# Optimization experiments

Hardware: AMD Instinct MI355X
Metric: run time of the kernel (lower is better)

Reference implementation:

```python
import jax, jax.numpy as jnp
import numpy as np
from jax import lax

ANG_RES = 9
MINDISP = -4
MAXDISP = 4
DN = ('NCHW', 'OIHW', 'NCHW')


def _dilat_pad(d, ang):
    if d < 0:
        dilat = abs(d) * ang + 1
        pad = (ang * (ang - 1) * abs(d)) // 2
    elif d == 0:
        dilat = 1
        pad = 0
    else:
        dilat = abs(d) * ang - 1
        pad = (ang * (ang - 1) * abs(d)) // 2 - ang + 1
    return dilat, pad


def setup_inputs() -> dict:
    key = jax.random.key(0)
    k1, k2 = jax.random.split(key)
    x = jax.random.normal(k1, (4, 64, 432, 432), dtype=jnp.float32)  # [B, Cin, angRes*H, angRes*W]
    W = jax.random.normal(k2, (64, 64, 9, 9), dtype=jnp.float32) * 0.05  # [Cout, Cin, angRes, angRes]
    return {"x": x, "W": W}


def reference(x, W):
    costs = []
    for d in range(MINDISP, MAXDISP + 1):
        dilat, pad = _dilat_pad(d, ANG_RES)
        cost = lax.conv_general_dilated(
            x, W,
            window_strides=(ANG_RES, ANG_RES),
            padding=[(pad, pad), (pad, pad)],
            rhs_dilation=(dilat, dilat),
            dimension_numbers=DN,
        )  # [B, Cout, H, W]
        costs.append(cost)
    # stack along new disparity axis -> [B, Cout, D, H, W]
    return jnp.stack(costs, axis=2)
```

## Files before the change

### kernel.cpp

```cpp
#include <hip/hip_runtime.h>

#define ANG 9
#define OHW 48
#define IMG 432
#define CIN 64
#define COUT 64
#define ND 9
#define NB 4
#define NVIEW 81
#define NSPAT 2304
#define NTOT 9216

#define SLABW 81
#define SLABSZ (80 * SLABW)

using f32x4 = __attribute__((ext_vector_type(4))) float;
using s16x8 = __attribute__((ext_vector_type(8))) short;

__device__ __forceinline__ unsigned short f2bf(float f) {
    unsigned u = __float_as_uint(f);
    unsigned r = (u + 0x7FFFu + ((u >> 16) & 1u)) >> 16;
    return (unsigned short)r;
}

__global__ void k_wpack(const float* __restrict__ w, unsigned short* __restrict__ aw) {
    int idx = blockIdx.x * 256 + threadIdx.x;
    if (idx >= NVIEW * 128 * 64) return;
    int ci = idx & 63;
    int m  = (idx >> 6) & 127;
    int uv = idx >> 13;
    int u = uv / 9, v = uv % 9;
    int co = m & 63, var = m >> 6;
    int uu = var ? 8 - u : u;
    int vv = var ? 8 - v : v;
    aw[idx] = f2bf(w[((size_t)(co * 64 + ci) * 9 + uu) * 9 + vv]);
}

__global__ __launch_bounds__(512, 4)
void k_fused(const float* __restrict__ x,
             const unsigned short* __restrict__ aw,
             unsigned short* __restrict__ y) {
    __shared__ unsigned short lx[IMG * 64];
    const int h = blockIdx.x, u = blockIdx.y, b = blockIdx.z;
    const int t = threadIdx.x;
    const int ih = 9 * h + u;
    const int lane = t & 63, wave = t >> 6;
    const int lr = lane & 15;
    const int lh = lane >> 4;
    const int mh = wave >> 2;
    const int mf = wave & 3;

    const unsigned short* abase =
        aw + (((size_t)(u * 9) * 128) + mh * 64 + mf * 16 + lr) * 64 + lh * 8;
    s16x8 a0[9];
#pragma unroll
    for (int v = 0; v < 9; ++v)
        a0[v] = *reinterpret_cast<const s16x8*>(abase + (size_t)v * 128 * 64);

    {
        const int tx = t & 127, ty = t >> 7;
        if (tx < 108) {
            const float* base = x + (((size_t)b * 64) * IMG + ih) * IMG + 4 * tx;
#pragma unroll 4
            for (int k = 0; k < 16; ++k) {
                const int ci = ty * 16 + k;
                const float4 v4 = *reinterpret_cast<const float4*>(
                    base + (size_t)ci * (IMG * IMG));
                unsigned short us[4] = {f2bf(v4.x), f2bf(v4.y), f2bf(v4.z), f2bf(v4.w)};
#pragma unroll
                for (int jj = 0; jj < 4; ++jj) {
                    const int iw = 4 * tx + jj;
                    const int sc = ci ^ (((iw >> 2) & 7) << 3);
                    lx[iw * 64 + sc] = us[jj];
                }
            }
        }
    }
    __syncthreads();

#pragma unroll
    for (int v = 0; v < 9; ++v) {
        const int uv = u * 9 + v;
        const s16x8 a1 = *reinterpret_cast<const s16x8*>(
            abase + (size_t)v * 128 * 64 + 32);
#pragma unroll
        for (int nt = 0; nt < 3; ++nt) {
            const int iw = 9 * (nt * 16 + lr) + v;
            const int g  = (iw >> 2) & 7;
            const s16x8 b0 = *reinterpret_cast<const s16x8*>(&lx[iw * 64 + ((lh ^ g) * 8)]);
            const s16x8 b1 = *reinterpret_cast<const s16x8*>(&lx[iw * 64 + (((4 + lh) ^ g) * 8)]);

            f32x4 acc = (f32x4){0.f, 0.f, 0.f, 0.f};
            acc = __builtin_amdgcn_mfma_f32_16x16x32_bf16(a0[v], b0, acc, 0, 0, 0);
            acc = __builtin_amdgcn_mfma_f32_16x16x32_bf16(a1,    b1, acc, 0, 0, 0);

            const int n0 = b * NSPAT + h * 48 + nt * 16;
#pragma unroll
            for (int rr = 0; rr < 4; ++rr) {
                const int m = mh * 64 + mf * 16 + lh * 4 + rr;
                y[((size_t)uv * 128 + m) * NTOT + n0 + lr] = f2bf(acc[rr]);
            }
        }
    }
}

__global__ __launch_bounds__(576)
void k_gather4(const unsigned short* __restrict__ y, float* __restrict__ out) {
    __shared__ float lds[2 * SLABSZ];
    const int co = blockIdx.x, b = blockIdx.y;
    const int tid = threadIdx.x;

    for (int i = tid; i < 2 * SLABSZ; i += 576) lds[i] = 0.f;

    const int var  = tid / 288;
    const int e0   = (tid % 288) * 8;
    const int srow = e0 / 48, scol = e0 % 48;
    const int ldst = var * SLABSZ + (16 + srow) * SLABW + 16 + scol;
    const unsigned short* ybase =
        y + ((size_t)(var * 64 + co)) * NTOT + (size_t)b * NSPAT + e0;

    const int hh = tid / 12;
    const int w0 = (tid % 12) * 4;
    const int center = (16 + hh) * SLABW + 16 + w0;

    float acc[9][4];
#pragma unroll
    for (int dd = 0; dd < 9; ++dd)
#pragma unroll
        for (int i = 0; i < 4; ++i) acc[dd][i] = 0.f;

    uint4 pre0 = *reinterpret_cast<const uint4*>(ybase);
    uint4 pre1 = *reinterpret_cast<const uint4*>(ybase + (size_t)128 * NTOT);
    __syncthreads();

    for (int uv = 0; uv < NVIEW; ++uv) {
        float4 lo, hi;
        lo.x = __uint_as_float(pre0.x << 16);
        lo.y = __uint_as_float(pre0.x & 0xffff0000u);
        lo.z = __uint_as_float(pre0.y << 16);
        lo.w = __uint_as_float(pre0.y & 0xffff0000u);
        hi.x = __uint_as_float(pre0.z << 16);
        hi.y = __uint_as_float(pre0.z & 0xffff0000u);
        hi.z = __uint_as_float(pre0.w << 16);
        hi.w = __uint_as_float(pre0.w & 0xffff0000u);
        *reinterpret_cast<float4*>(&lds[ldst])     = lo;
        *reinterpret_cast<float4*>(&lds[ldst + 4]) = hi;

        pre0 = pre1;
        if (uv + 2 < NVIEW)
            pre1 = *reinterpret_cast<const uint4*>(ybase + (size_t)(uv + 2) * 128 * NTOT);

        __syncthreads();

        const int uq = uv / 9, vq = uv % 9;
        const int step = (uq - 4) * SLABW + (vq - 4);
        int base = center + 4 * step;
#pragma unroll
        for (int dd = 0; dd < 9; ++dd) {
            const float* p = &lds[base + (dd > 4 ? SLABSZ : 0)];
            acc[dd][0] += p[0];
            acc[dd][1] += p[1];
            acc[dd][2] += p[2];
            acc[dd][3] += p[3];
            base -= step;
        }
        __syncthreads();
    }

    const size_t ob = (size_t)(b * 64 + co) * 9 * NSPAT + tid * 4;
#pragma unroll
    for (int dd = 0; dd < 9; ++dd) {
        float4 o;
        o.x = acc[dd][0]; o.y = acc[dd][1]; o.z = acc[dd][2]; o.w = acc[dd][3];
        *reinterpret_cast<float4*>(&out[ob + (size_t)dd * NSPAT]) = o;
    }
}

__global__ __launch_bounds__(192)
void cost_volume_direct(const float* __restrict__ x,
                        const float* __restrict__ w,
                        float* __restrict__ out) {
    const int ow      = threadIdx.x;
    const int oh      = blockIdx.y * 4 + threadIdx.y;
    const int co_tile = blockIdx.x & 7;
    const int dd      = blockIdx.x >> 3;
    const int b       = blockIdx.z;
    const int d       = dd - 4;
    const int co0     = co_tile * 8;

    int dilat, pad;
    if (d < 0)       { dilat = (-d) * ANG + 1; pad = 36 * (-d); }
    else if (d == 0) { dilat = 1;              pad = 0; }
    else             { dilat = d * ANG - 1;    pad = 36 * d - (ANG - 1); }

    const int ih0 = oh * ANG - pad;
    const int iw0 = ow * ANG - pad;

    float acc[8];
#pragma unroll
    for (int i = 0; i < 8; ++i) acc[i] = 0.f;

    const float* xb = x + (size_t)b * CIN * IMG * IMG;
    for (int kh = 0; kh < ANG; ++kh) {
        const int ih = ih0 + kh * dilat;
        if ((unsigned)ih >= (unsigned)IMG) continue;
        const float* xrow_base = xb + (size_t)ih * IMG;
        const float* wrow      = w + kh * ANG;
        for (int ci = 0; ci < CIN; ++ci) {
            const float* xrow = xrow_base + (size_t)ci * (IMG * IMG);
            float xv[ANG];
#pragma unroll
            for (int kw = 0; kw < ANG; ++kw) {
                const int iw  = iw0 + kw * dilat;
                const bool ok = ((unsigned)iw < (unsigned)IMG);
                const float vv = xrow[ok ? iw : 0];
                xv[kw] = ok ? vv : 0.f;
            }
            const float* wc = wrow + ci * (ANG * ANG);
#pragma unroll
            for (int i = 0; i < 8; ++i) {
                const float* wi = wc + (size_t)(co0 + i) * (CIN * ANG * ANG);
#pragma unroll
                for (int kw = 0; kw < ANG; ++kw)
                    acc[i] = fmaf(xv[kw], wi[kw], acc[i]);
            }
        }
    }
#pragma unroll
    for (int i = 0; i < 8; ++i) {
        const size_t o = ((((size_t)b * COUT + (co0 + i)) * ND + dd) * OHW + oh) * OHW + ow;
        out[o] = acc[i];
    }
}

extern "C" void kernel_launch(void* const* d_in, const int* in_sizes, int n_in,
                              void* d_out, int out_size, void* d_ws, size_t ws_size,
                              hipStream_t stream) {
    const float* x   = (const float*)d_in[0];
    const float* w   = (const float*)d_in[1];
    float*       out = (float*)d_out;

    const size_t AW_BYTES = (size_t)NVIEW * 128 * 64 * 2;
    const size_t Y_BYTES  = (size_t)NVIEW * 128 * NTOT * 2;
    const size_t NEED     = AW_BYTES + Y_BYTES;

    if (ws_size >= NEED) {
        unsigned short* aw = (unsigned short*)d_ws;
        unsigned short* yb = (unsigned short*)((char*)d_ws + AW_BYTES);

        k_wpack  <<<dim3((NVIEW * 128 * 64 + 255) / 256), dim3(256), 0, stream>>>(w, aw);
        k_fused  <<<dim3(OHW, ANG, NB), dim3(512), 0, stream>>>(x, aw, yb);
        k_gather4<<<dim3(COUT, NB), dim3(576), 0, stream>>>(yb, out);
    } else {
        dim3 grid(8 * ND, OHW / 4, NB);
        dim3 block(OHW, 4, 1);
        cost_volume_direct<<<grid, block, 0, stream>>>(x, w, out);
    }
}
```

Measured before the change: 223.4 us.

## Split gather by variant across blocks, double-buffer slabs, repack LDS input layout

The gather kernel now runs each weight variant (negative and positive disparities) in a separate block. This doubles the grid and halves the per-thread accumulators, and double-buffered slabs remove one barrier per view. The fused MFMA kernel stages input with per-wave coalesced scalar loads of 4 channels packed into 64-bit LDS stores. That LDS layout is padded instead of XOR-swizzled, and the next view's A fragment is prefetched. The aim is more gather parallelism and fewer stalls and bank conflicts, at the cost of more redundant slab zeroing and staging traffic.

```diff
diff --git a/kernel.cpp b/kernel.cpp
--- a/kernel.cpp
+++ b/kernel.cpp
@@ -14,8 +14,11 @@
 #define SLABW 81
 #define SLABSZ (80 * SLABW)
 
+#define LXW 68
+
 using f32x4 = __attribute__((ext_vector_type(4))) float;
 using s16x8 = __attribute__((ext_vector_type(8))) short;
+using s16x4 = __attribute__((ext_vector_type(4))) short;
 
 __device__ __forceinline__ unsigned short f2bf(float f) {
     unsigned u = __float_as_uint(f);
@@ -40,7 +43,7 @@
 void k_fused(const float* __restrict__ x,
              const unsigned short* __restrict__ aw,
              unsigned short* __restrict__ y) {
-    __shared__ unsigned short lx[IMG * 64];
+    __shared__ unsigned short lx[IMG * LXW];
     const int h = blockIdx.x, u = blockIdx.y, b = blockIdx.z;
     const int t = threadIdx.x;
     const int ih = 9 * h + u;
@@ -58,37 +61,47 @@
         a0[v] = *reinterpret_cast<const s16x8*>(abase + (size_t)v * 128 * 64);
 
     {
-        const int tx = t & 127, ty = t >> 7;
-        if (tx < 108) {
-            const float* base = x + (((size_t)b * 64) * IMG + ih) * IMG + 4 * tx;
-#pragma unroll 4
-            for (int k = 0; k < 16; ++k) {
-                const int ci = ty * 16 + k;
-                const float4 v4 = *reinterpret_cast<const float4*>(
-                    base + (size_t)ci * (IMG * IMG));
-                unsigned short us[4] = {f2bf(v4.x), f2bf(v4.y), f2bf(v4.z), f2bf(v4.w)};
-#pragma unroll
-                for (int jj = 0; jj < 4; ++jj) {
-                    const int iw = 4 * tx + jj;
-                    const int sc = ci ^ (((iw >> 2) & 7) << 3);
-                    lx[iw * 64 + sc] = us[jj];
-                }
+        const size_t xrow = ((size_t)b * 64) * (IMG * IMG) + (size_t)ih * IMG;
+        for (int task = wave; task < 112; task += 8) {
+            const int cg = task / 7;
+            const int ch = task % 7;
+            const int iw = ch * 64 + lane;
+            if (iw < IMG) {
+                const float* p = x + xrow + (size_t)(cg * 4) * (IMG * IMG) + iw;
+                const float f0 = p[0];
+                const float f1 = p[(size_t)(IMG * IMG)];
+                const float f2 = p[(size_t)(2 * IMG * IMG)];
+                const float f3 = p[(size_t)(3 * IMG * IMG)];
+                const unsigned long long pk =
+                      (unsigned long long)f2bf(f0)
+                    | ((unsigned long long)f2bf(f1) << 16)
+                    | ((unsigned long long)f2bf(f2) << 32)
+                    | ((unsigned long long)f2bf(f3) << 48);
+                reinterpret_cast<unsigned long long*>(lx)[iw * (LXW / 4) + cg] = pk;
             }
         }
     }
     __syncthreads();
 
+    const s16x4* lx4 = reinterpret_cast<const s16x4*>(lx);
+
+    s16x8 a1n = *reinterpret_cast<const s16x8*>(abase + 32);
 #pragma unroll
     for (int v = 0; v < 9; ++v) {
         const int uv = u * 9 + v;
-        const s16x8 a1 = *reinterpret_cast<const s16x8*>(
-            abase + (size_t)v * 128 * 64 + 32);
+        const s16x8 a1 = a1n;
+        if (v < 8)
+            a1n = *reinterpret_cast<const s16x8*>(abase + (size_t)(v + 1) * 128 * 64 + 32);
 #pragma unroll
         for (int nt = 0; nt < 3; ++nt) {
             const int iw = 9 * (nt * 16 + lr) + v;
-            const int g  = (iw >> 2) & 7;
-            const s16x8 b0 = *reinterpret_cast<const s16x8*>(&lx[iw * 64 + ((lh ^ g) * 8)]);
-            const s16x8 b1 = *reinterpret_cast<const s16x8*>(&lx[iw * 64 + (((4 + lh) ^ g) * 8)]);
+            const int r0 = iw * (LXW / 4) + 2 * lh;
+            const s16x4 p0 = lx4[r0];
+            const s16x4 p1 = lx4[r0 + 1];
+            const s16x4 p2 = lx4[r0 + 8];
+            const s16x4 p3 = lx4[r0 + 9];
+            const s16x8 b0 = __builtin_shufflevector(p0, p1, 0, 1, 2, 3, 4, 5, 6, 7);
+            const s16x8 b1 = __builtin_shufflevector(p2, p3, 0, 1, 2, 3, 4, 5, 6, 7);
 
             f32x4 acc = (f32x4){0.f, 0.f, 0.f, 0.f};
             acc = __builtin_amdgcn_mfma_f32_16x16x32_bf16(a0[v], b0, acc, 0, 0, 0);
@@ -105,74 +118,78 @@
 }
 
 __global__ __launch_bounds__(576)
-void k_gather4(const unsigned short* __restrict__ y, float* __restrict__ out) {
-    __shared__ float lds[2 * SLABSZ];
-    const int co = blockIdx.x, b = blockIdx.y;
+void k_gather5(const unsigned short* __restrict__ y, float* __restrict__ out) {
+    __shared__ float lds[2][SLABSZ];
+    const int co = blockIdx.x, b = blockIdx.y, var = blockIdx.z;
     const int tid = threadIdx.x;
 
-    for (int i = tid; i < 2 * SLABSZ; i += 576) lds[i] = 0.f;
-
-    const int var  = tid / 288;
+    for (int i = tid; i < 2 * SLABSZ; i += 576) ((float*)lds)[i] = 0.f;
+
+    const bool stg = (tid < 288);
     const int e0   = (tid % 288) * 8;
     const int srow = e0 / 48, scol = e0 % 48;
-    const int ldst = var * SLABSZ + (16 + srow) * SLABW + 16 + scol;
+    const int ldst = (16 + srow) * SLABW + 16 + scol;
     const unsigned short* ybase =
         y + ((size_t)(var * 64 + co)) * NTOT + (size_t)b * NSPAT + e0;
 
     const int hh = tid / 12;
     const int w0 = (tid % 12) * 4;
     const int center = (16 + hh) * SLABW + 16 + w0;
-
-    float acc[9][4];
-#pragma unroll
-    for (int dd = 0; dd < 9; ++dd)
-#pragma unroll
-        for (int i = 0; i < 4; ++i) acc[dd][i] = 0.f;
-
-    uint4 pre0 = *reinterpret_cast<const uint4*>(ybase);
-    uint4 pre1 = *reinterpret_cast<const uint4*>(ybase + (size_t)128 * NTOT);
+    const int kmax = var ? 4 : 5;
+
+    float acc[5][4] = {};
+
+    uint4 pre0, pre1;
+    if (stg) {
+        pre0 = *reinterpret_cast<const uint4*>(ybase);
+        pre1 = *reinterpret_cast<const uint4*>(ybase + (size_t)128 * NTOT);
+    }
     __syncthreads();
 
     for (int uv = 0; uv < NVIEW; ++uv) {
-        float4 lo, hi;
-        lo.x = __uint_as_float(pre0.x << 16);
-        lo.y = __uint_as_float(pre0.x & 0xffff0000u);
-        lo.z = __uint_as_float(pre0.y << 16);
-        lo.w = __uint_as_float(pre0.y & 0xffff0000u);
-        hi.x = __uint_as_float(pre0.z << 16);
-        hi.y = __uint_as_float(pre0.z & 0xffff0000u);
-        hi.z = __uint_as_float(pre0.w << 16);
-        hi.w = __uint_as_float(pre0.w & 0xffff0000u);
-        *reinterpret_cast<float4*>(&lds[ldst])     = lo;
-        *reinterpret_cast<float4*>(&lds[ldst + 4]) = hi;
-
-        pre0 = pre1;
-        if (uv + 2 < NVIEW)
-            pre1 = *reinterpret_cast<const uint4*>(ybase + (size_t)(uv + 2) * 128 * NTOT);
-
+        float* slab = lds[uv & 1];
+        if (stg) {
+            float4 lo, hi;
+            lo.x = __uint_as_float(pre0.x << 16);
+            lo.y = __uint_as_float(pre0.x & 0xffff0000u);
+            lo.z = __uint_as_float(pre0.y << 16);
+            lo.w = __uint_as_float(pre0.y & 0xffff0000u);
+            hi.x = __uint_as_float(pre0.z << 16);
+            hi.y = __uint_as_float(pre0.z & 0xffff0000u);
+            hi.z = __uint_as_float(pre0.w << 16);
+            hi.w = __uint_as_float(pre0.w & 0xffff0000u);
+            *reinterpret_cast<float4*>(&slab[ldst])     = lo;
+            *reinterpret_cast<float4*>(&slab[ldst + 4]) = hi;
+            pre0 = pre1;
+            if (uv + 2 < NVIEW)
+                pre1 = *reinterpret_cast<const uint4*>(ybase + (size_t)(uv + 2) * 128 * NTOT);
+        }
         __syncthreads();
 
         const int uq = uv / 9, vq = uv % 9;
         const int step = (uq - 4) * SLABW + (vq - 4);
-        int base = center + 4 * step;
-#pragma unroll
-        for (int dd = 0; dd < 9; ++dd) {
-            const float* p = &lds[base + (dd > 4 ? SLABSZ : 0)];
-            acc[dd][0] += p[0];
-            acc[dd][1] += p[1];
-            acc[dd][2] += p[2];
-            acc[dd][3] += p[3];
-            base -= step;
-        }
-        __syncthreads();
-    }
-
-    const size_t ob = (size_t)(b * 64 + co) * 9 * NSPAT + tid * 4;
-#pragma unroll
-    for (int dd = 0; dd < 9; ++dd) {
-        float4 o;
-        o.x = acc[dd][0]; o.y = acc[dd][1]; o.z = acc[dd][2]; o.w = acc[dd][3];
-        *reinterpret_cast<float4*>(&out[ob + (size_t)dd * NSPAT]) = o;
+#pragma unroll
+        for (int k = 0; k < 5; ++k) {
+            if (k < kmax) {
+                const int mult = var ? (-1 - k) : (4 - k);
+                const float* p = &slab[center + mult * step];
+                acc[k][0] += p[0];
+                acc[k][1] += p[1];
+                acc[k][2] += p[2];
+                acc[k][3] += p[3];
+            }
+        }
+    }
+
+    const int ddb = var ? 5 : 0;
+    const size_t ob = ((size_t)(b * 64 + co) * 9 + ddb) * NSPAT + tid * 4;
+#pragma unroll
+    for (int k = 0; k < 5; ++k) {
+        if (k < kmax) {
+            float4 o;
+            o.x = acc[k][0]; o.y = acc[k][1]; o.z = acc[k][2]; o.w = acc[k][3];
+            *reinterpret_cast<float4*>(&out[ob + (size_t)k * NSPAT]) = o;
+        }
     }
 }
 
@@ -250,7 +267,7 @@
 
         k_wpack  <<<dim3((NVIEW * 128 * 64 + 255) / 256), dim3(256), 0, stream>>>(w, aw);
         k_fused  <<<dim3(OHW, ANG, NB), dim3(512), 0, stream>>>(x, aw, yb);
-        k_gather4<<<dim3(COUT, NB), dim3(576), 0, stream>>>(yb, out);
+        k_gather5<<<dim3(COUT, NB, 2), dim3(576), 0, stream>>>(yb, out);
     } else {
         dim3 grid(8 * ND, OHW / 4, NB);
         dim3 block(OHW, 4, 1);
```

Result: slower. 272.5 us (+22.0%).

## Split fused conv kernel across width thirds with smaller padded LDS tile

Applied to the files above, without the earlier changes.

The fused kernel's grid now splits each input row into three 144-pixel width tiles, giving three times as many blocks, and cuts LDS from a full 432x64 row to a 144x68 padded tile. Staging now loads four channels per thread as scalar floats and writes them packed as 64-bit words into a padded layout that replaces the XOR swizzle. The weight operand for the next view is prefetched one iteration ahead. The intent is more occupancy and parallelism, at the cost of strided scalar global loads and re-reading the A weights in each tile block.

```diff
diff --git a/kernel.cpp b/kernel.cpp
--- a/kernel.cpp
+++ b/kernel.cpp
@@ -14,8 +14,12 @@
 #define SLABW 81
 #define SLABSZ (80 * SLABW)
 
+#define NIW 144
+#define LXW 68
+
 using f32x4 = __attribute__((ext_vector_type(4))) float;
 using s16x8 = __attribute__((ext_vector_type(8))) short;
+using s16x4 = __attribute__((ext_vector_type(4))) short;
 
 __device__ __forceinline__ unsigned short f2bf(float f) {
     unsigned u = __float_as_uint(f);
@@ -40,8 +44,10 @@
 void k_fused(const float* __restrict__ x,
              const unsigned short* __restrict__ aw,
              unsigned short* __restrict__ y) {
-    __shared__ unsigned short lx[IMG * 64];
-    const int h = blockIdx.x, u = blockIdx.y, b = blockIdx.z;
+    __shared__ unsigned short lx[NIW * LXW];
+    const int wtu = blockIdx.x;
+    const int wt  = wtu % 3, u = wtu / 3;
+    const int h = blockIdx.y, b = blockIdx.z;
     const int t = threadIdx.x;
     const int ih = 9 * h + u;
     const int lane = t & 63, wave = t >> 6;
@@ -58,48 +64,81 @@
         a0[v] = *reinterpret_cast<const s16x8*>(abase + (size_t)v * 128 * 64);
 
     {
-        const int tx = t & 127, ty = t >> 7;
-        if (tx < 108) {
-            const float* base = x + (((size_t)b * 64) * IMG + ih) * IMG + 4 * tx;
-#pragma unroll 4
-            for (int k = 0; k < 16; ++k) {
-                const int ci = ty * 16 + k;
-                const float4 v4 = *reinterpret_cast<const float4*>(
-                    base + (size_t)ci * (IMG * IMG));
-                unsigned short us[4] = {f2bf(v4.x), f2bf(v4.y), f2bf(v4.z), f2bf(v4.w)};
-#pragma unroll
-                for (int jj = 0; jj < 4; ++jj) {
-                    const int iw = 4 * tx + jj;
-                    const int sc = ci ^ (((iw >> 2) & 7) << 3);
-                    lx[iw * 64 + sc] = us[jj];
-                }
-            }
+        const size_t xbase = ((size_t)b * 64) * (IMG * IMG) + (size_t)ih * IMG
+                           + (size_t)(wt * NIW);
+        float f[5][4];
+#pragma unroll
+        for (int k = 0; k < 4; ++k) {
+            const int id = t + 512 * k;
+            const int cg = id / NIW, il = id % NIW;
+            const float* p = x + xbase + (size_t)(4 * cg) * (IMG * IMG) + il;
+            f[k][0] = p[0];
+            f[k][1] = p[(size_t)(IMG * IMG)];
+            f[k][2] = p[(size_t)(2 * IMG * IMG)];
+            f[k][3] = p[(size_t)(3 * IMG * IMG)];
+        }
+        if (t < 256) {
+            const int id = 2048 + t;
+            const int cg = id / NIW, il = id % NIW;
+            const float* p = x + xbase + (size_t)(4 * cg) * (IMG * IMG) + il;
+            f[4][0] = p[0];
+            f[4][1] = p[(size_t)(IMG * IMG)];
+            f[4][2] = p[(size_t)(2 * IMG * IMG)];
+            f[4][3] = p[(size_t)(3 * IMG * IMG)];
+        }
+        unsigned long long* lx64 = reinterpret_cast<unsigned long long*>(lx);
+#pragma unroll
+        for (int k = 0; k < 4; ++k) {
+            const int id = t + 512 * k;
+            const int cg = id / NIW, il = id % NIW;
+            const unsigned long long pk =
+                  (unsigned long long)f2bf(f[k][0])
+                | ((unsigned long long)f2bf(f[k][1]) << 16)
+                | ((unsigned long long)f2bf(f[k][2]) << 32)
+                | ((unsigned long long)f2bf(f[k][3]) << 48);
+            lx64[il * 17 + cg] = pk;
+        }
+        if (t < 256) {
+            const int id = 2048 + t;
+            const int cg = id / NIW, il = id % NIW;
+            const unsigned long long pk =
+                  (unsigned long long)f2bf(f[4][0])
+                | ((unsigned long long)f2bf(f[4][1]) << 16)
+                | ((unsigned long long)f2bf(f[4][2]) << 32)
+                | ((unsigned long long)f2bf(f[4][3]) << 48);
+            lx64[il * 17 + cg] = pk;
         }
     }
     __syncthreads();
 
+    const s16x4* lx4 = reinterpret_cast<const s16x4*>(lx);
+    const int n0 = b * NSPAT + h * 48 + wt * 16;
+
+    s16x8 a1n = *reinterpret_cast<const s16x8*>(abase + 32);
 #pragma unroll
     for (int v = 0; v < 9; ++v) {
         const int uv = u * 9 + v;
-        const s16x8 a1 = *reinterpret_cast<const s16x8*>(
-            abase + (size_t)v * 128 * 64 + 32);
-#pragma unroll
-        for (int nt = 0; nt < 3; ++nt) {
-            const int iw = 9 * (nt * 16 + lr) + v;
-            const int g  = (iw >> 2) & 7;
-            const s16x8 b0 = *reinterpret_cast<const s16x8*>(&lx[iw * 64 + ((lh ^ g) * 8)]);
-            const s16x8 b1 = *reinterpret_cast<const s16x8*>(&lx[iw * 64 + (((4 + lh) ^ g) * 8)]);
-
-            f32x4 acc = (f32x4){0.f, 0.f, 0.f, 0.f};
-            acc = __builtin_amdgcn_mfma_f32_16x16x32_bf16(a0[v], b0, acc, 0, 0, 0);
-            acc = __builtin_amdgcn_mfma_f32_16x16x32_bf16(a1,    b1, acc, 0, 0, 0);
-
-            const int n0 = b * NSPAT + h * 48 + nt * 16;
-#pragma unroll
-            for (int rr = 0; rr < 4; ++rr) {
-                const int m = mh * 64 + mf * 16 + lh * 4 + rr;
-                y[((size_t)uv * 128 + m) * NTOT + n0 + lr] = f2bf(acc[rr]);
-            }
+        const s16x8 a1 = a1n;
+        if (v < 8)
+            a1n = *reinterpret_cast<const s16x8*>(abase + (size_t)(v + 1) * 128 * 64 + 32);
+
+        const int iwl = 9 * lr + v;
+        const int r0  = iwl * 17 + 2 * lh;
+        const s16x4 p0 = lx4[r0];
+        const s16x4 p1 = lx4[r0 + 1];
+        const s16x4 p2 = lx4[r0 + 8];
+        const s16x4 p3 = lx4[r0 + 9];
+        const s16x8 b0 = __builtin_shufflevector(p0, p1, 0, 1, 2, 3, 4, 5, 6, 7);
+        const s16x8 b1 = __builtin_shufflevector(p2, p3, 0, 1, 2, 3, 4, 5, 6, 7);
+
+        f32x4 acc = (f32x4){0.f, 0.f, 0.f, 0.f};
+        acc = __builtin_amdgcn_mfma_f32_16x16x32_bf16(a0[v], b0, acc, 0, 0, 0);
+        acc = __builtin_amdgcn_mfma_f32_16x16x32_bf16(a1,    b1, acc, 0, 0, 0);
+
+#pragma unroll
+        for (int rr = 0; rr < 4; ++rr) {
+            const int m = mh * 64 + mf * 16 + lh * 4 + rr;
+            y[((size_t)uv * 128 + m) * NTOT + n0 + lr] = f2bf(acc[rr]);
         }
     }
 }
@@ -249,7 +288,7 @@
         unsigned short* yb = (unsigned short*)((char*)d_ws + AW_BYTES);
 
         k_wpack  <<<dim3((NVIEW * 128 * 64 + 255) / 256), dim3(256), 0, stream>>>(w, aw);
-        k_fused  <<<dim3(OHW, ANG, NB), dim3(512), 0, stream>>>(x, aw, yb);
+        k_fused  <<<dim3(27, OHW, NB), dim3(512), 0, stream>>>(x, aw, yb);
         k_gather4<<<dim3(COUT, NB), dim3(576), 0, stream>>>(yb, out);
     } else {
         dim3 grid(8 * ND, OHW / 4, NB);
```

Result: slower. 331.4 us (+48.3%).
